# Optimization experiments

Hardware: AMD Instinct MI355X
Metric: run time of the kernel (lower is better)

## Reference

```python
import jax, jax.numpy as jnp
import numpy as np

NUM_F = 5
POLY = 3
GRID_LO, GRID_HI = -1.0, 1.0


def _ext_grid():
    # 6-point grid on [-1, 1], extended by POLY knots on each side (pykan B_batch extend)
    g = np.linspace(GRID_LO, GRID_HI, NUM_F + 1)
    h = (GRID_HI - GRID_LO) / NUM_F
    left = g[0] - h * np.arange(POLY, 0, -1)
    right = g[-1] + h * np.arange(1, POLY + 1)
    return jnp.asarray(np.concatenate([left, g, right]), dtype=jnp.float32)  # (12,)


def bspline_basis(x, grid, k):
    # Cox-de Boor recursion; x: (...,), grid: (G,) shared knots -> (..., G-1-k)
    x1 = x[..., None]
    B = ((x1 >= grid[:-1]) & (x1 < grid[1:])).astype(x.dtype)
    for d in range(1, k + 1):
        left = (x1 - grid[:-(d + 1)]) / (grid[d:-1] - grid[:-(d + 1)])
        right = (grid[d + 1:] - x1) / (grid[d + 1:] - grid[1:-d])
        B = left * B[..., :-1] + right * B[..., 1:]
    return B


def setup_inputs():
    key = jax.random.key(0)
    ks = jax.random.split(key, 5)
    batch, heads, patches, dim, out_dim = 8, 4, 64, 8, 8
    act_in = heads * patches * dim    # 2048
    act_out = heads * patches * out_dim  # 2048
    N = act_in * act_out              # 4_194_304 spline edges
    C = NUM_F + POLY                  # 8 coefficients per edge
    return {
        "q": jax.random.normal(ks[0], (batch, heads, patches, dim), jnp.float32),
        "k": jax.random.normal(ks[1], (batch, heads, patches, dim), jnp.float32),
        "coef_q": jax.random.normal(ks[2], (N, C), jnp.float32) * 0.05,
        "coef_k": jax.random.normal(ks[3], (N, C), jnp.float32) * 0.05,
        "scale_base": jnp.ones((N,), jnp.float32),
        "scale_sp": jnp.ones((N,), jnp.float32),
        "mask_q": jnp.ones((N,), jnp.float32),
        "mask_k": jnp.ones((N,), jnp.float32),
        "bias_w": jax.random.normal(ks[4], (2048,), jnp.float32) * 0.02,
    }


def reference(q, k, coef_q, coef_k, scale_base, scale_sp, mask_q, mask_k, bias_w):
    batch, heads, patches, dim = q.shape
    act_in = heads * patches * dim
    act_out = bias_w.shape[0]
    out_dim = act_out // (heads * patches)
    C = NUM_F + POLY
    grid = _ext_grid()

    xq = q.reshape(batch, act_in)
    xk = k.reshape(batch, act_in)
    Bq = bspline_basis(xq, grid, POLY)  # (batch, act_in, C)
    Bk = bspline_basis(xk, grid, POLY)

    def branch(x, B, coef, mask):
        # edge activation f[o,i](x_i) = mask*(scale_base*silu(x_i) + scale_sp*spline_{o,i}(x_i)),
        # reduced over all act_in inputs -> (batch, act_out)
        sb = (mask * scale_base).reshape(act_out, act_in)
        sp = (mask * scale_sp).reshape(act_out, act_in)
        base = jax.nn.silu(x)  # (batch, act_in)
        y = jnp.einsum('bi,oi->bo', base, sb)
        y = y + jnp.einsum('bic,oic,oi->bo', B, coef.reshape(act_out, act_in, C), sp)
        return y

    y = branch(xq, Bq, coef_q, mask_q) + branch(xk, Bk, coef_k, mask_k)
    y = y.reshape(batch, heads, patches, out_dim) + bias_w.reshape(1, heads, patches, out_dim)
    return jax.nn.softmax(y, axis=-1)
```

## Files before the change

kernel.cpp:

```cpp
#include <hip/hip_runtime.h>
#include <math.h>


#define ACT 2048
#define BATCH 8
#define IBLK 64
#define NIC (ACT / IBLK)
#define OBLK 64
#define NOC (ACT / OBLK)

__device__ __forceinline__ float dot4(const float4& a, const float4& b) {
  float r = a.x * b.x;
  r = fmaf(a.y, b.y, r);
  r = fmaf(a.z, b.z, r);
  r = fmaf(a.w, b.w, r);
  return r;
}

__global__ void kan_precompute(const float* __restrict__ q, const float* __restrict__ k,
                               float4* __restrict__ Bq, float4* __restrict__ Bk,
                               float* __restrict__ baseq, float* __restrict__ basek) {
  int tid = blockIdx.x * blockDim.x + threadIdx.x;
  if (tid >= ACT * BATCH) return;
  int il = tid & (IBLK - 1);
  int b = (tid >> 6) & 7;
  int ic = tid >> 9;
  int i = ic * IBLK + il;
  const float t0 = -2.2f;
  const float h = 0.4f;
  for (int br = 0; br < 2; ++br) {
    const float* xsrc = br ? k : q;
    float4* Bdst = br ? Bk : Bq;
    float* basedst = br ? basek : baseq;
    float x = xsrc[(size_t)b * ACT + i];
    float Bv[11];
#pragma unroll
    for (int j = 0; j < 11; ++j) {
      float tj = t0 + h * (float)j;
      float tj1 = t0 + h * (float)(j + 1);
      Bv[j] = (x >= tj && x < tj1) ? 1.0f : 0.0f;
    }
#pragma unroll
    for (int d = 1; d <= 3; ++d) {
      float inv = 1.0f / (h * (float)d);
#pragma unroll
      for (int j = 0; j + d < 11; ++j) {
        float tj = t0 + h * (float)j;
        float tjd1 = t0 + h * (float)(j + d + 1);
        Bv[j] = (x - tj) * inv * Bv[j] + (tjd1 - x) * inv * Bv[j + 1];
      }
    }
    Bdst[((size_t)ic * 16 + b * 2 + 0) * IBLK + il] = make_float4(Bv[0], Bv[1], Bv[2], Bv[3]);
    Bdst[((size_t)ic * 16 + b * 2 + 1) * IBLK + il] = make_float4(Bv[4], Bv[5], Bv[6], Bv[7]);
    basedst[((size_t)ic * 8 + b) * IBLK + il] = x / (1.0f + expf(-x));
  }
}

__global__ __launch_bounds__(512, 8) void kan_main(
    const float* __restrict__ coef_q, const float* __restrict__ coef_k,
    const float* __restrict__ scale_base, const float* __restrict__ scale_sp,
    const float* __restrict__ mask_q, const float* __restrict__ mask_k,
    const float4* __restrict__ Bq, const float4* __restrict__ Bk,
    const float* __restrict__ baseq, const float* __restrict__ basek,
    float* __restrict__ y_part) {
  __shared__ float4 BsQ[16 * IBLK];
  __shared__ float4 BsK[16 * IBLK];
  __shared__ float basQ[8 * IBLK];
  __shared__ float basK[8 * IBLK];

  const int t = threadIdx.x;
  const int l = t & 63;
  const int w = t >> 6;
  const int oc = blockIdx.x >> 5;
  const int ic = blockIdx.x & 31;
  const int o0 = oc * OBLK;
  const size_t ibase = (size_t)ic * IBLK + l;

  {
    const float4* srcq = Bq + (size_t)ic * 16 * IBLK;
    const float4* srck = Bk + (size_t)ic * 16 * IBLK;
#pragma unroll
    for (int r = 0; r < 2; ++r) {
      BsQ[r * 512 + t] = srcq[r * 512 + t];
      BsK[r * 512 + t] = srck[r * 512 + t];
    }
    if (t < 128) {
      reinterpret_cast<float4*>(basQ)[t] =
          reinterpret_cast<const float4*>(baseq + (size_t)ic * 8 * IBLK)[t];
    } else if (t < 256) {
      reinterpret_cast<float4*>(basK)[t - 128] =
          reinterpret_cast<const float4*>(basek + (size_t)ic * 8 * IBLK)[t - 128];
    }
  }
  __syncthreads();

#pragma unroll 1
  for (int s = 0; s < 8; ++s) {
    const int oa = o0 + s * 8 + w;
    const size_t e = (size_t)oa * ACT + ibase;

    const float4* cpq = reinterpret_cast<const float4*>(coef_q + e * 8);
    const float4* cpk = reinterpret_cast<const float4*>(coef_k + e * 8);
    float4 cq0 = cpq[0], cq1 = cpq[1];
    float4 ck0 = cpk[0], ck1 = cpk[1];
    float mq = mask_q[e], mk = mask_k[e];
    float sb = scale_base[e], ss = scale_sp[e];

    float vbq = mq * sb, vsq = mq * ss, vbk = mk * sb, vsk = mk * ss;

    float acc[BATCH];
#pragma unroll
    for (int b = 0; b < BATCH; ++b) {
      const float4 Bq0 = BsQ[(b * 2 + 0) * IBLK + l];
      const float4 Bq1 = BsQ[(b * 2 + 1) * IBLK + l];
      float dq = dot4(Bq0, cq0) + dot4(Bq1, cq1);
      const float4 Bk0 = BsK[(b * 2 + 0) * IBLK + l];
      const float4 Bk1 = BsK[(b * 2 + 1) * IBLK + l];
      float dk = dot4(Bk0, ck0) + dot4(Bk1, ck1);
      const float bsq = basQ[b * IBLK + l];
      const float bsk = basK[b * IBLK + l];
      float a = vsq * dq;
      a = fmaf(vsk, dk, a);
      a = fmaf(vbq, bsq, a);
      a = fmaf(vbk, bsk, a);
      acc[b] = a;
      __builtin_amdgcn_sched_barrier(0);
    }

#pragma unroll
    for (int b = 0; b < BATCH; ++b) {
#pragma unroll
      for (int off = 1; off < 8; off <<= 1) acc[b] += __shfl_xor(acc[b], off);
    }
    float v = acc[0];
#pragma unroll
    for (int b = 1; b < BATCH; ++b) v = ((l & 7) == b) ? acc[b] : v;
#pragma unroll
    for (int off = 8; off < 64; off <<= 1) v += __shfl_xor(v, off);

    if (l < 8) y_part[(size_t)oa * (NIC * 8) + ic * 8 + l] = v;
  }
}

__global__ void kan_softmax(const float* __restrict__ y_part,
                            const float* __restrict__ bias,
                            float* __restrict__ out) {
  const int t = threadIdx.x;
  const int wid = blockIdx.x * 4 + (t >> 6);
  const int b = wid >> 8;
  const int grp = wid & 255;
  const int l = t & 63;
  const int op = l >> 3;
  const int sub = l & 7;
  const int o = grp * 8 + op;

  float p = 0.0f;
#pragma unroll
  for (int j = 0; j < 4; ++j) {
    int icc = sub + 8 * j;
    p += y_part[(size_t)o * (NIC * 8) + icc * 8 + b];
  }
#pragma unroll
  for (int off = 1; off < 8; off <<= 1) p += __shfl_xor(p, off);
  float v = p + bias[o];
  float m = v;
#pragma unroll
  for (int off = 8; off < 64; off <<= 1) m = fmaxf(m, __shfl_xor(m, off));
  float e = expf(v - m);
  float ssum = e;
#pragma unroll
  for (int off = 8; off < 64; off <<= 1) ssum += __shfl_xor(ssum, off);
  if (sub == 0) out[(size_t)b * ACT + o] = e / ssum;
}

extern "C" void kernel_launch(void* const* d_in, const int* in_sizes, int n_in,
                              void* d_out, int out_size, void* d_ws, size_t ws_size,
                              hipStream_t stream) {
  const float* q          = (const float*)d_in[0];
  const float* k          = (const float*)d_in[1];
  const float* coef_q     = (const float*)d_in[2];
  const float* coef_k     = (const float*)d_in[3];
  const float* scale_base = (const float*)d_in[4];
  const float* scale_sp   = (const float*)d_in[5];
  const float* mask_q     = (const float*)d_in[6];
  const float* mask_k     = (const float*)d_in[7];
  const float* bias_w     = (const float*)d_in[8];
  float* out = (float*)d_out;

  float* ws     = (float*)d_ws;
  float* y_part = ws;
  float* Bq     = ws + 524288;
  float* Bk     = Bq + 131072;
  float* baseq  = Bk + 131072;
  float* basek  = baseq + 16384;

  kan_precompute<<<dim3(64), dim3(256), 0, stream>>>(
      q, k, (float4*)Bq, (float4*)Bk, baseq, basek);
  kan_main<<<dim3(NOC * NIC), dim3(512), 0, stream>>>(
      coef_q, coef_k, scale_base, scale_sp, mask_q, mask_k,
      (const float4*)Bq, (const float4*)Bk, baseq, basek, y_part);
  kan_softmax<<<dim3(512), dim3(256), 0, stream>>>(y_part, bias_w, out);
}
```

Measured before the change: 83.70 us.

## Process two outputs per wave with packed FMA and butterfly transpose reduction

Each wave now handles two adjacent output rows per iteration, using packed two-wide FMAs over the shared B-spline values. The mask and scale factors are folded into the coefficients before the batch loop, which cuts per-batch multiplies. The shuffle reduction becomes a butterfly-transpose that reduces eight batch accumulators with fewer shuffles, and the softmax kernel reads the results using the new bit-permuted slot order. This raises register use and changes the floating-point summation order.

Measured after the change: 84.17 us. No clear change (+0.6%).

```diff
diff --git a/kernel.cpp b/kernel.cpp
--- a/kernel.cpp
+++ b/kernel.cpp
@@ -9,11 +9,15 @@
 #define OBLK 64
 #define NOC (ACT / OBLK)
 
-__device__ __forceinline__ float dot4(const float4& a, const float4& b) {
-  float r = a.x * b.x;
-  r = fmaf(a.y, b.y, r);
-  r = fmaf(a.z, b.z, r);
-  r = fmaf(a.w, b.w, r);
+typedef float v2f __attribute__((ext_vector_type(2)));
+
+__device__ __forceinline__ v2f fma2(v2f a, v2f b, v2f c) {
+  return __builtin_elementwise_fma(a, b, c);
+}
+__device__ __forceinline__ v2f shflx2(v2f v, int m) {
+  v2f r;
+  r.x = __shfl_xor(v.x, m);
+  r.y = __shfl_xor(v.y, m);
   return r;
 }
 
@@ -95,50 +99,131 @@
   __syncthreads();
 
 #pragma unroll 1
-  for (int s = 0; s < 8; ++s) {
-    const int oa = o0 + s * 8 + w;
-    const size_t e = (size_t)oa * ACT + ibase;
-
-    const float4* cpq = reinterpret_cast<const float4*>(coef_q + e * 8);
-    const float4* cpk = reinterpret_cast<const float4*>(coef_k + e * 8);
-    float4 cq0 = cpq[0], cq1 = cpq[1];
-    float4 ck0 = cpk[0], ck1 = cpk[1];
-    float mq = mask_q[e], mk = mask_k[e];
-    float sb = scale_base[e], ss = scale_sp[e];
-
-    float vbq = mq * sb, vsq = mq * ss, vbk = mk * sb, vsk = mk * ss;
-
-    float acc[BATCH];
+  for (int s = 0; s < 4; ++s) {
+    const int oa = o0 + w * 8 + s * 2;
+    const size_t e0 = (size_t)oa * ACT + ibase;
+    const size_t e1 = e0 + ACT;
+
+    v2f acc2[BATCH];
+#pragma unroll
+    for (int b = 0; b < BATCH; ++b) acc2[b] = (v2f){0.0f, 0.0f};
+
+    float mq0 = mask_q[e0], mq1 = mask_q[e1];
+    float mk0 = mask_k[e0], mk1 = mask_k[e1];
+    float sb0 = scale_base[e0], sb1 = scale_base[e1];
+    float ss0 = scale_sp[e0], ss1 = scale_sp[e1];
+    v2f vbq = {mq0 * sb0, mq1 * sb1};
+    v2f vbk = {mk0 * sb0, mk1 * sb1};
+    v2f vsq = {mq0 * ss0, mq1 * ss1};
+    v2f vsk = {mk0 * ss0, mk1 * ss1};
+
+    v2f cs[8];
+    {
+      const float4* c0p = reinterpret_cast<const float4*>(coef_q + e0 * 8);
+      const float4* c1p = reinterpret_cast<const float4*>(coef_q + e1 * 8);
+      float4 a0 = c0p[0], a1 = c0p[1];
+      float4 b0 = c1p[0], b1 = c1p[1];
+      cs[0] = (v2f){a0.x, b0.x} * vsq;
+      cs[1] = (v2f){a0.y, b0.y} * vsq;
+      cs[2] = (v2f){a0.z, b0.z} * vsq;
+      cs[3] = (v2f){a0.w, b0.w} * vsq;
+      cs[4] = (v2f){a1.x, b1.x} * vsq;
+      cs[5] = (v2f){a1.y, b1.y} * vsq;
+      cs[6] = (v2f){a1.z, b1.z} * vsq;
+      cs[7] = (v2f){a1.w, b1.w} * vsq;
+    }
 #pragma unroll
     for (int b = 0; b < BATCH; ++b) {
-      const float4 Bq0 = BsQ[(b * 2 + 0) * IBLK + l];
-      const float4 Bq1 = BsQ[(b * 2 + 1) * IBLK + l];
-      float dq = dot4(Bq0, cq0) + dot4(Bq1, cq1);
-      const float4 Bk0 = BsK[(b * 2 + 0) * IBLK + l];
-      const float4 Bk1 = BsK[(b * 2 + 1) * IBLK + l];
-      float dk = dot4(Bk0, ck0) + dot4(Bk1, ck1);
-      const float bsq = basQ[b * IBLK + l];
-      const float bsk = basK[b * IBLK + l];
-      float a = vsq * dq;
-      a = fmaf(vsk, dk, a);
-      a = fmaf(vbq, bsq, a);
-      a = fmaf(vbk, bsk, a);
-      acc[b] = a;
+      const float4 B0 = BsQ[(b * 2 + 0) * IBLK + l];
+      const float4 B1 = BsQ[(b * 2 + 1) * IBLK + l];
+      const float bs = basQ[b * IBLK + l];
+      v2f a = acc2[b];
+      a = fma2(cs[0], (v2f){B0.x, B0.x}, a);
+      a = fma2(cs[1], (v2f){B0.y, B0.y}, a);
+      a = fma2(cs[2], (v2f){B0.z, B0.z}, a);
+      a = fma2(cs[3], (v2f){B0.w, B0.w}, a);
+      a = fma2(cs[4], (v2f){B1.x, B1.x}, a);
+      a = fma2(cs[5], (v2f){B1.y, B1.y}, a);
+      a = fma2(cs[6], (v2f){B1.z, B1.z}, a);
+      a = fma2(cs[7], (v2f){B1.w, B1.w}, a);
+      a = fma2(vbq, (v2f){bs, bs}, a);
+      acc2[b] = a;
       __builtin_amdgcn_sched_barrier(0);
     }
-
+    {
+      const float4* c0p = reinterpret_cast<const float4*>(coef_k + e0 * 8);
+      const float4* c1p = reinterpret_cast<const float4*>(coef_k + e1 * 8);
+      float4 a0 = c0p[0], a1 = c0p[1];
+      float4 b0 = c1p[0], b1 = c1p[1];
+      cs[0] = (v2f){a0.x, b0.x} * vsk;
+      cs[1] = (v2f){a0.y, b0.y} * vsk;
+      cs[2] = (v2f){a0.z, b0.z} * vsk;
+      cs[3] = (v2f){a0.w, b0.w} * vsk;
+      cs[4] = (v2f){a1.x, b1.x} * vsk;
+      cs[5] = (v2f){a1.y, b1.y} * vsk;
+      cs[6] = (v2f){a1.z, b1.z} * vsk;
+      cs[7] = (v2f){a1.w, b1.w} * vsk;
+    }
 #pragma unroll
     for (int b = 0; b < BATCH; ++b) {
-#pragma unroll
-      for (int off = 1; off < 8; off <<= 1) acc[b] += __shfl_xor(acc[b], off);
-    }
-    float v = acc[0];
-#pragma unroll
-    for (int b = 1; b < BATCH; ++b) v = ((l & 7) == b) ? acc[b] : v;
-#pragma unroll
-    for (int off = 8; off < 64; off <<= 1) v += __shfl_xor(v, off);
-
-    if (l < 8) y_part[(size_t)oa * (NIC * 8) + ic * 8 + l] = v;
+      const float4 B0 = BsK[(b * 2 + 0) * IBLK + l];
+      const float4 B1 = BsK[(b * 2 + 1) * IBLK + l];
+      const float bs = basK[b * IBLK + l];
+      v2f a = acc2[b];
+      a = fma2(cs[0], (v2f){B0.x, B0.x}, a);
+      a = fma2(cs[1], (v2f){B0.y, B0.y}, a);
+      a = fma2(cs[2], (v2f){B0.z, B0.z}, a);
+      a = fma2(cs[3], (v2f){B0.w, B0.w}, a);
+      a = fma2(cs[4], (v2f){B1.x, B1.x}, a);
+      a = fma2(cs[5], (v2f){B1.y, B1.y}, a);
+      a = fma2(cs[6], (v2f){B1.z, B1.z}, a);
+      a = fma2(cs[7], (v2f){B1.w, B1.w}, a);
+      a = fma2(vbk, (v2f){bs, bs}, a);
+      acc2[b] = a;
+      __builtin_amdgcn_sched_barrier(0);
+    }
+
+    v2f n0, n1, n2, n3;
+    {
+      const bool hi = (l & 1);
+      v2f s0 = hi ? acc2[0] : acc2[4];
+      v2f s1 = hi ? acc2[1] : acc2[5];
+      v2f s2 = hi ? acc2[2] : acc2[6];
+      v2f s3 = hi ? acc2[3] : acc2[7];
+      v2f k0 = hi ? acc2[4] : acc2[0];
+      v2f k1 = hi ? acc2[5] : acc2[1];
+      v2f k2 = hi ? acc2[6] : acc2[2];
+      v2f k3 = hi ? acc2[7] : acc2[3];
+      n0 = k0 + shflx2(s0, 1);
+      n1 = k1 + shflx2(s1, 1);
+      n2 = k2 + shflx2(s2, 1);
+      n3 = k3 + shflx2(s3, 1);
+    }
+    v2f m0, m1;
+    {
+      const bool hi = (l & 2);
+      v2f s0 = hi ? n0 : n2;
+      v2f s1 = hi ? n1 : n3;
+      v2f k0 = hi ? n2 : n0;
+      v2f k1 = hi ? n3 : n1;
+      m0 = k0 + shflx2(s0, 2);
+      m1 = k1 + shflx2(s1, 2);
+    }
+    v2f r;
+    {
+      const bool hi = (l & 4);
+      v2f s0 = hi ? m0 : m1;
+      v2f k0 = hi ? m1 : m0;
+      r = k0 + shflx2(s0, 4);
+    }
+    r = r + shflx2(r, 8);
+    r = r + shflx2(r, 16);
+    r = r + shflx2(r, 32);
+
+    if (l < 8) {
+      y_part[(size_t)oa * (NIC * 8) + ic * 8 + l] = r.x;
+      y_part[(size_t)(oa + 1) * (NIC * 8) + ic * 8 + l] = r.y;
+    }
   }
 }
 
@@ -153,12 +238,13 @@
   const int op = l >> 3;
   const int sub = l & 7;
   const int o = grp * 8 + op;
+  const int slot = ((b & 1) << 2) | (b & 2) | ((b >> 2) & 1);
 
   float p = 0.0f;
 #pragma unroll
   for (int j = 0; j < 4; ++j) {
     int icc = sub + 8 * j;
-    p += y_part[(size_t)o * (NIC * 8) + icc * 8 + b];
+    p += y_part[(size_t)o * (NIC * 8) + icc * 8 + slot];
   }
 #pragma unroll
   for (int off = 1; off < 8; off <<= 1) p += __shfl_xor(p, off);
```
